# Kernel optimization log

Measured on AMD Instinct MI355X. Metric: run time of the kernel, lower is better.

The kernel has to match this reference:

```python
import jax, jax.numpy as jnp
import numpy as np

B, S, HID = 2, 1024, 1024
H, P, D = 16, 2, 64
SCALE = 1.0 / np.sqrt(D)


def setup_inputs() -> dict:
    key = jax.random.key(0)
    ks = jax.random.split(key, 9)
    hidden_states = jax.random.normal(ks[0], (B, S, HID), dtype=jnp.float32)
    w_std = 0.02
    Wq = jax.random.normal(ks[1], (HID, HID), dtype=jnp.float32) * w_std
    Wk = jax.random.normal(ks[2], (HID, HID), dtype=jnp.float32) * w_std
    Wv = jax.random.normal(ks[3], (HID, HID), dtype=jnp.float32) * w_std
    Wo = jax.random.normal(ks[4], (HID, HID), dtype=jnp.float32) * w_std
    # alpha_* initialized as identity over heads, broadcast over pseudo dim, plus noise
    ident = jnp.broadcast_to(jnp.eye(H, dtype=jnp.float32)[:, :, None], (H, H, P))
    alpha_q = ident + 0.01 * jax.random.normal(ks[5], (H, H, P), dtype=jnp.float32)
    alpha_k = ident + 0.01 * jax.random.normal(ks[6], (H, H, P), dtype=jnp.float32)
    alpha_v = ident + 0.01 * jax.random.normal(ks[7], (H, H, P), dtype=jnp.float32)
    # collapse: (H, H*P), one-hot picking pseudo-head 0 of each head, plus noise
    collapse = jnp.zeros((H, H * P), dtype=jnp.float32)
    hi = jnp.arange(H)
    collapse = collapse.at[hi, hi * P].set(1.0)
    collapse = collapse + 0.01 * jax.random.normal(ks[8], (H, H * P), dtype=jnp.float32)
    return {"hidden_states": hidden_states, "Wq": Wq, "Wk": Wk, "Wv": Wv, "Wo": Wo,
            "alpha_q": alpha_q, "alpha_k": alpha_k, "alpha_v": alpha_v, "collapse": collapse}


def _iha_forward(x, Wq, Wk, Wv, Wo, alpha_q, alpha_k, alpha_v, collapse):
    b, s, _ = x.shape
    # projections (torch F.linear: x @ W^T), split into heads -> (b, H, s, D)
    def proj(W):
        return jnp.einsum('bse,fe->bsf', x, W).reshape(b, s, H, D).transpose(0, 2, 1, 3)
    q, k, v = proj(Wq), proj(Wk), proj(Wv)
    # head mixing: mhp,bmnd->bhpnd then merge pseudo into virtual seq (b,H,s*P,D)
    def mix_merge(alpha, t):
        t = jnp.einsum('mhp,bmnd->bhpnd', alpha, t)
        return t.transpose(0, 1, 3, 2, 4).reshape(b, H, s * P, D)
    q, k, v = mix_merge(alpha_q, q), mix_merge(alpha_k, k), mix_merge(alpha_v, v)
    # causal SDPA over virtual positions
    sv = s * P
    scores = jnp.einsum('bhqd,bhkd->bhqk', q, k) * jnp.asarray(SCALE, x.dtype)
    vpos = jnp.arange(sv)
    causal = vpos[:, None] >= vpos[None, :]
    scores = jnp.where(causal, scores, jnp.asarray(-jnp.inf, x.dtype))
    probs = jax.nn.softmax(scores, axis=-1)
    attn = jnp.einsum('bhqk,bhkd->bhqd', probs, v)  # (b, H, sv, D)
    # collapse pseudo heads: (b,H,s,P,D) -> (b,s,H*P,D) -> einsum with collapse
    attn = attn.reshape(b, H, s, P, D).transpose(0, 2, 1, 3, 4).reshape(b, s, H * P, D)
    attn = jnp.einsum('ho,bnod->bhnd', collapse, attn)  # (b, H, s, D)
    attn = attn.transpose(0, 2, 1, 3).reshape(b, s, HID)
    return jnp.einsum('bse,fe->bsf', attn, Wo)


def reference(hidden_states, Wq, Wk, Wv, Wo, alpha_q, alpha_k, alpha_v, collapse):
    return _iha_forward(hidden_states, Wq, Wk, Wv, Wo, alpha_q, alpha_k, alpha_v, collapse)
```

## Files before the change

kernel.cpp:

```cpp
#include <hip/hip_runtime.h>
#include <hip/hip_bf16.h>

#define B_    2
#define S_    1024
#define HID_  1024
#define H_    16
#define P_    2
#define D_    64
#define SV_   2048
#define NBH_  32
#define SCALE_LOG2E 0.18033688f

typedef __attribute__((ext_vector_type(8))) short short8;
typedef __attribute__((ext_vector_type(4))) short short4b;
typedef __attribute__((ext_vector_type(4))) float f32x4;

#if __has_builtin(__builtin_amdgcn_exp2f)
#define EXP2(x) __builtin_amdgcn_exp2f(x)
#else
#define EXP2(x) exp2f(x)
#endif

__device__ __forceinline__ unsigned short f2bf(float f) {
  union { float f; unsigned u; } v; v.f = f;
  unsigned r = v.u + 0x7fffu + ((v.u >> 16) & 1u);
  return (unsigned short)(r >> 16);
}
__device__ __forceinline__ unsigned pack_bf2(float a, float b) {
  __hip_bfloat162 h = __float22bfloat162_rn(make_float2(a, b));
  unsigned u; __builtin_memcpy(&u, &h, 4);
  return u;
}

__global__ __launch_bounds__(256) void cast_f32_bf16(
    const float* __restrict__ src, unsigned short* __restrict__ dst, int n4) {
  int i = blockIdx.x * blockDim.x + threadIdx.x;
  int stride = gridDim.x * blockDim.x;
  for (; i < n4; i += stride) {
    float4 v = ((const float4*)src)[i];
    ushort4 o;
    o.x = f2bf(v.x); o.y = f2bf(v.y); o.z = f2bf(v.z); o.w = f2bf(v.w);
    ((ushort4*)dst)[i] = o;
  }
}

__global__ __launch_bounds__(256) void weff_kernel(
    const float* __restrict__ Wq, const float* __restrict__ Wk,
    const float* __restrict__ Wv,
    const float* __restrict__ aq, const float* __restrict__ ak,
    const float* __restrict__ av,
    unsigned short* __restrict__ Weff) {
  __shared__ float Al[16][32];
  const int d = blockIdx.x;
  const int t = blockIdx.y;
  const float* W = (t == 0) ? Wq : ((t == 1) ? Wk : Wv);
  const float* A = (t == 0) ? aq : ((t == 1) ? ak : av);
  const int tid = threadIdx.x;
  for (int idx = tid; idx < 512; idx += 256) Al[idx >> 5][idx & 31] = A[idx];
  __syncthreads();
  const int e = tid * 4;
  float wr[16][4];
#pragma unroll
  for (int m = 0; m < 16; ++m) {
    float4 v = *(const float4*)(W + (size_t)(m * 64 + d) * 1024 + e);
    wr[m][0] = v.x; wr[m][1] = v.y; wr[m][2] = v.z; wr[m][3] = v.w;
  }
  for (int hp = 0; hp < 32; ++hp) {
    float acc0 = 0.f, acc1 = 0.f, acc2 = 0.f, acc3 = 0.f;
#pragma unroll
    for (int m = 0; m < 16; ++m) {
      float al = Al[m][hp];
      acc0 += al * wr[m][0]; acc1 += al * wr[m][1];
      acc2 += al * wr[m][2]; acc3 += al * wr[m][3];
    }
    int r = (hp >> 1) * 128 + (hp & 1) * 64 + d;
    ushort4 ov;
    ov.x = f2bf(acc0); ov.y = f2bf(acc1); ov.z = f2bf(acc2); ov.w = f2bf(acc3);
    *(ushort4*)(Weff + ((size_t)t * 2048 + r) * 1024 + e) = ov;
  }
}

__global__ __launch_bounds__(256) void woeff_kernel(
    const float* __restrict__ Wo, const float* __restrict__ coll,
    unsigned short* __restrict__ Woeff) {
  __shared__ float wrow[1024];
  __shared__ float cl[512];
  const int f = blockIdx.x;
  const int tid = threadIdx.x;
  for (int idx = tid; idx < 512; idx += 256) cl[idx] = coll[idx];
  for (int idx = tid; idx < 1024; idx += 256) wrow[idx] = Wo[(size_t)f * 1024 + idx];
  __syncthreads();
  for (int idx = tid; idx < 2048; idx += 256) {
    int o = idx >> 6, d = idx & 63;
    float acc = 0.f;
#pragma unroll
    for (int h = 0; h < 16; ++h) acc += wrow[h * 64 + d] * cl[h * 32 + o];
    Woeff[(size_t)f * 2048 + idx] = f2bf(acc);
  }
}

__global__ __launch_bounds__(512) void qkv_gemm256(
    const unsigned short* __restrict__ Xb,
    const unsigned short* __restrict__ Weff,
    unsigned short* __restrict__ Qd, unsigned short* __restrict__ Kd,
    unsigned short* __restrict__ Vd) {
  __shared__ unsigned short As[3][256 * 64];
  __shared__ unsigned short Bs[2][256 * 64];
  constexpr int K = 1024;
  constexpr int NT = 16;
  const int t = threadIdx.x;
  const int wave = t >> 6, lane = t & 63, lrow = lane & 15, quad = lane >> 4;
  const int wm = wave >> 2, wn = wave & 3;
  const int z = blockIdx.z;
  const int row0 = blockIdx.x * 256, col0 = blockIdx.y * 256;
  const unsigned short* Ap = (z == 2) ? (Weff + (size_t)2 * 2048 * 1024) : Xb;
  const unsigned short* Bp = (z == 2) ? Xb : (Weff + (size_t)z * 2048 * 1024);

  const int srow8 = lane >> 3;
  const int sslot = (lane & 7) ^ srow8;

  auto stageHT = [&](const unsigned short* __restrict__ gsrc,
                     unsigned short* __restrict__ ldsbase,
                     int half, int kt, int trow0) {
#pragma unroll
    for (int j = 0; j < 2; ++j) {
      const int rloc = half * 128 + wave * 16 + j * 8;
      const unsigned short* g =
          gsrc + (size_t)(trow0 + rloc + srow8) * K + kt * 64 + sslot * 8;
      __builtin_amdgcn_global_load_lds(
          (const __attribute__((address_space(1))) unsigned int*)g,
          (__attribute__((address_space(3))) unsigned int*)(ldsbase + rloc * 64),
          16, 0, 0);
    }
  };

  f32x4 acc[8][4];
#pragma unroll
  for (int mi = 0; mi < 8; ++mi)
#pragma unroll
    for (int ni = 0; ni < 4; ++ni) acc[mi][ni] = (f32x4){0.f, 0.f, 0.f, 0.f};

  stageHT(Ap, &As[0][0], 0, 0, row0);
  stageHT(Ap, &As[0][0], 1, 0, row0);
  stageHT(Bp, &Bs[0][0], 0, 0, col0);
  stageHT(Bp, &Bs[0][0], 1, 0, col0);
  stageHT(Ap, &As[1][0], 0, 1, row0);
  stageHT(Ap, &As[1][0], 1, 1, row0);
  stageHT(Bp, &Bs[1][0], 0, 1, col0);
  stageHT(Bp, &Bs[1][0], 1, 1, col0);
  asm volatile("s_waitcnt vmcnt(8)" ::: "memory");
  asm volatile("s_barrier" ::: "memory");

  const int swz = lrow & 7;

#define LDA(mi, ks)                                                         \
  (*(const short8*)(Ab + (wm * 128 + (mi)*16 + lrow) * 64 +                 \
                    ((((ks)*4 + quad) ^ swz) * 8)))

#define MFMA_PAIR(mA, mB, a00, a01, a10, a11)                               \
  _Pragma("unroll") for (int ni = 0; ni < 4; ++ni) {                        \
    acc[mA][ni] = __builtin_amdgcn_mfma_f32_16x16x32_bf16(                  \
        a00, bfrag[ni][0], acc[mA][ni], 0, 0, 0);                           \
    acc[mA][ni] = __builtin_amdgcn_mfma_f32_16x16x32_bf16(                  \
        a01, bfrag[ni][1], acc[mA][ni], 0, 0, 0);                           \
    acc[mB][ni] = __builtin_amdgcn_mfma_f32_16x16x32_bf16(                  \
        a10, bfrag[ni][0], acc[mB][ni], 0, 0, 0);                           \
    acc[mB][ni] = __builtin_amdgcn_mfma_f32_16x16x32_bf16(                  \
        a11, bfrag[ni][1], acc[mB][ni], 0, 0, 0);                           \
  }

  for (int kt = 0; kt < NT; ++kt) {
    const int abuf = kt % 3;
    const int anext = (kt + 2) % 3;
    const int bbuf = kt & 1;
    const bool pf = (kt + 2 < NT);
    const unsigned short* __restrict__ Ab = &As[abuf][0];
    const unsigned short* __restrict__ Bb = &Bs[bbuf][0];

    short8 bfrag[4][2];
    {
#pragma unroll
      for (int ni = 0; ni < 4; ++ni) {
        const int R = wn * 64 + ni * 16 + lrow;
#pragma unroll
        for (int ks = 0; ks < 2; ++ks)
          bfrag[ni][ks] =
              *(const short8*)(Bb + R * 64 + (((ks * 4 + quad) ^ swz) * 8));
      }
      short8 a00 = LDA(0, 0), a01 = LDA(0, 1), a10 = LDA(1, 0), a11 = LDA(1, 1);
      if (pf) stageHT(Ap, &As[anext][0], 0, kt + 2, row0);
      asm volatile("s_barrier" ::: "memory");
      asm volatile("s_waitcnt lgkmcnt(0)" ::: "memory");
      __builtin_amdgcn_s_setprio(1);
      MFMA_PAIR(0, 1, a00, a01, a10, a11)
      __builtin_amdgcn_s_setprio(0);
      asm volatile("s_barrier" ::: "memory");
    }
    {
      short8 a00 = LDA(2, 0), a01 = LDA(2, 1), a10 = LDA(3, 0), a11 = LDA(3, 1);
      if (pf) stageHT(Ap, &As[anext][0], 1, kt + 2, row0);
      asm volatile("s_barrier" ::: "memory");
      asm volatile("s_waitcnt lgkmcnt(0)" ::: "memory");
      __builtin_amdgcn_s_setprio(1);
      MFMA_PAIR(2, 3, a00, a01, a10, a11)
      __builtin_amdgcn_s_setprio(0);
      asm volatile("s_barrier" ::: "memory");
    }
    {
      short8 a00 = LDA(4, 0), a01 = LDA(4, 1), a10 = LDA(5, 0), a11 = LDA(5, 1);
      if (pf) stageHT(Bp, &Bs[bbuf][0], 0, kt + 2, col0);
      asm volatile("s_barrier" ::: "memory");
      asm volatile("s_waitcnt lgkmcnt(0)" ::: "memory");
      __builtin_amdgcn_s_setprio(1);
      MFMA_PAIR(4, 5, a00, a01, a10, a11)
      __builtin_amdgcn_s_setprio(0);
      asm volatile("s_barrier" ::: "memory");
    }
    {
      short8 a00 = LDA(6, 0), a01 = LDA(6, 1), a10 = LDA(7, 0), a11 = LDA(7, 1);
      if (pf) stageHT(Bp, &Bs[bbuf][0], 1, kt + 2, col0);
      asm volatile("s_barrier" ::: "memory");
      asm volatile("s_waitcnt lgkmcnt(0)" ::: "memory");
      __builtin_amdgcn_s_setprio(1);
      MFMA_PAIR(6, 7, a00, a01, a10, a11)
      __builtin_amdgcn_s_setprio(0);
      if (pf) {
        asm volatile("s_waitcnt vmcnt(8)" ::: "memory");
      } else {
        asm volatile("s_waitcnt vmcnt(0)" ::: "memory");
      }
      asm volatile("s_barrier" ::: "memory");
    }
  }
#undef LDA
#undef MFMA_PAIR

#pragma unroll
  for (int mi = 0; mi < 8; ++mi) {
#pragma unroll
    for (int ni = 0; ni < 4; ++ni) {
#pragma unroll
      for (int i = 0; i < 4; ++i) {
        int grow = row0 + wm * 128 + mi * 16 + quad * 4 + i;
        int gcol = col0 + wn * 64 + ni * 16 + lrow;
        float val = acc[mi][ni][i];
        if (z != 2) {
          if (z == 0) val *= SCALE_LOG2E;
          int b = grow >> 10, n = grow & 1023;
          int h = gcol >> 7, p = (gcol >> 6) & 1, d = gcol & 63;
          unsigned short* dst = (z == 0) ? Qd : Kd;
          dst[((size_t)((b * 16 + h) * 2048) + n * 2 + p) * 64 + d] = f2bf(val);
        } else {
          int h = grow >> 7, p = (grow >> 6) & 1, d = grow & 63;
          int b = gcol >> 10, n = gcol & 1023;
          Vd[((size_t)((b * 16 + h) * 64 + d)) * 2048 + n * 2 + p] = f2bf(val);
        }
      }
    }
  }
}

__global__ __launch_bounds__(256) void gemm64p(
    const unsigned short* __restrict__ A,
    const unsigned short* __restrict__ Bbase,
    float* __restrict__ Cf) {
  __shared__ unsigned short As[3][64 * 64];
  __shared__ unsigned short Bs[3][64 * 64];
  constexpr int K = 2048, N = 1024, NT = 32;
  const int t = threadIdx.x;
  const int wave = t >> 6, lane = t & 63, lrow = lane & 15, quad = lane >> 4;
  const int wm = wave >> 1, wn = wave & 1;
  const int row0 = blockIdx.x * 64, col0 = blockIdx.y * 64;
  const int srow8 = lane >> 3;
  const int sslot = (lane & 7) ^ srow8;
  const int swz = lrow & 7;

  auto stage = [&](int kt, int buf) {
#pragma unroll
    for (int j = 0; j < 2; ++j) {
      const int rloc = wave * 16 + j * 8;
      const unsigned short* ga =
          A + (size_t)(row0 + rloc + srow8) * K + kt * 64 + sslot * 8;
      __builtin_amdgcn_global_load_lds(
          (const __attribute__((address_space(1))) unsigned int*)ga,
          (__attribute__((address_space(3))) unsigned int*)(&As[buf][rloc * 64]),
          16, 0, 0);
      const unsigned short* gb =
          Bbase + (size_t)(col0 + rloc + srow8) * K + kt * 64 + sslot * 8;
      __builtin_amdgcn_global_load_lds(
          (const __attribute__((address_space(1))) unsigned int*)gb,
          (__attribute__((address_space(3))) unsigned int*)(&Bs[buf][rloc * 64]),
          16, 0, 0);
    }
  };

  f32x4 acc[2][2];
#pragma unroll
  for (int mi = 0; mi < 2; ++mi)
#pragma unroll
    for (int ni = 0; ni < 2; ++ni) acc[mi][ni] = (f32x4){0.f, 0.f, 0.f, 0.f};

  stage(0, 0);
  stage(1, 1);

  for (int kt = 0; kt < NT; ++kt) {
    const int buf = kt % 3;
    if (kt < NT - 1) {
      asm volatile("s_waitcnt vmcnt(4)" ::: "memory");
    } else {
      asm volatile("s_waitcnt vmcnt(0)" ::: "memory");
    }
    asm volatile("s_barrier" ::: "memory");
    if (kt + 2 < NT) stage(kt + 2, (kt + 2) % 3);

    const unsigned short* __restrict__ Ab = &As[buf][0];
    const unsigned short* __restrict__ Bb = &Bs[buf][0];
    short8 af[2][2], bf[2][2];
#pragma unroll
    for (int mi = 0; mi < 2; ++mi)
#pragma unroll
      for (int ks = 0; ks < 2; ++ks)
        af[mi][ks] = *(const short8*)(
            Ab + (wm * 32 + mi * 16 + lrow) * 64 + (((ks * 4 + quad) ^ swz) * 8));
#pragma unroll
    for (int ni = 0; ni < 2; ++ni)
#pragma unroll
      for (int ks = 0; ks < 2; ++ks)
        bf[ni][ks] = *(const short8*)(
            Bb + (wn * 32 + ni * 16 + lrow) * 64 + (((ks * 4 + quad) ^ swz) * 8));
    __builtin_amdgcn_s_setprio(1);
#pragma unroll
    for (int mi = 0; mi < 2; ++mi)
#pragma unroll
      for (int ni = 0; ni < 2; ++ni) {
        acc[mi][ni] = __builtin_amdgcn_mfma_f32_16x16x32_bf16(
            af[mi][0], bf[ni][0], acc[mi][ni], 0, 0, 0);
        acc[mi][ni] = __builtin_amdgcn_mfma_f32_16x16x32_bf16(
            af[mi][1], bf[ni][1], acc[mi][ni], 0, 0, 0);
      }
    __builtin_amdgcn_s_setprio(0);
  }

#pragma unroll
  for (int mi = 0; mi < 2; ++mi)
#pragma unroll
    for (int ni = 0; ni < 2; ++ni)
#pragma unroll
      for (int i = 0; i < 4; ++i) {
        int grow = row0 + wm * 32 + mi * 16 + quad * 4 + i;
        int gcol = col0 + wn * 32 + ni * 16 + lrow;
        Cf[(size_t)grow * N + gcol] = acc[mi][ni][i];
      }
}

__global__ __launch_bounds__(256, 3) void attn_kernel(
    const unsigned short* __restrict__ Qv, const unsigned short* __restrict__ Kv,
    const unsigned short* __restrict__ Vt, unsigned short* __restrict__ Aov) {
  __shared__ unsigned short Ks[3][4096];
  __shared__ unsigned short Vs[3][4096];
  const int bh = blockIdx.x;
  const int yy = blockIdx.y;
  const int qt = (yy < 16) ? yy : (47 - yy);
  const int t = threadIdx.x;
  const int w = t >> 6, lane = t & 63, lq = lane & 15, quad = lane >> 4;
  const int l3 = lq & 7;

  const unsigned short* Qh = Qv + (size_t)bh * SV_ * D_;
  const unsigned short* Kh = Kv + (size_t)bh * SV_ * D_;
  const unsigned short* Vh = Vt + (size_t)bh * D_ * SV_;

  const int qrow = qt * 64 + w * 16 + lq;
  short8 bq0 = *(const short8*)(Qh + (size_t)qrow * 64 + quad * 8);
  short8 bq1 = *(const short8*)(Qh + (size_t)qrow * 64 + 32 + quad * 8);

  const int sg = (lane & 7) ^ ((lane >> 3) & 7);
  const int r0 = w * 16 + (lane >> 3);
  const unsigned short* Kg0 = Kh + r0 * 64 + sg * 8;
  const unsigned short* Vg0 = Vh + (size_t)r0 * SV_ + sg * 8;
  const int lds0 = w * 1024;
  const int lds1 = lds0 + 512;

  auto stage = [&](int kt) {
    const int buf = kt % 3;
    const unsigned short* kg = Kg0 + kt * 4096;
    const unsigned short* vg = Vg0 + kt * 64;
    __builtin_amdgcn_global_load_lds(
        (const __attribute__((address_space(1))) unsigned int*)kg,
        (__attribute__((address_space(3))) unsigned int*)(&Ks[buf][lds0]), 16, 0, 0);
    __builtin_amdgcn_global_load_lds(
        (const __attribute__((address_space(1))) unsigned int*)(kg + 8 * 64),
        (__attribute__((address_space(3))) unsigned int*)(&Ks[buf][lds1]), 16, 0, 0);
    __builtin_amdgcn_global_load_lds(
        (const __attribute__((address_space(1))) unsigned int*)vg,
        (__attribute__((address_space(3))) unsigned int*)(&Vs[buf][lds0]), 16, 0, 0);
    __builtin_amdgcn_global_load_lds(
        (const __attribute__((address_space(1))) unsigned int*)(vg + (size_t)8 * SV_),
        (__attribute__((address_space(3))) unsigned int*)(&Vs[buf][lds1]), 16, 0, 0);
  };

  float l_sum = 0.f;
  f32x4 o_acc[4];
#pragma unroll
  for (int nd = 0; nd < 4; ++nd) o_acc[nd] = (f32x4){0.f, 0.f, 0.f, 0.f};

  const int nt = qt + 1;
  stage(0);
  if (nt > 1) stage(1);

  for (int kt = 0; kt < nt; ++kt) {
    const int buf = kt % 3;
    if (kt + 1 < nt) {
      asm volatile("s_waitcnt vmcnt(4)" ::: "memory");
    } else {
      asm volatile("s_waitcnt vmcnt(0)" ::: "memory");
    }
    asm volatile("s_barrier" ::: "memory");
    if (kt + 2 < nt) stage(kt + 2);

    const unsigned short* Kb = Ks[buf];
    short8 ka[4][2];
#pragma unroll
    for (int t4 = 0; t4 < 4; ++t4)
#pragma unroll
      for (int c = 0; c < 2; ++c)
        ka[t4][c] = *(const short8*)(Kb + (t4 * 16 + lq) * 64 + (((c * 4 + quad) ^ l3) * 8));

    f32x4 s[4];
#pragma unroll
    for (int t4 = 0; t4 < 4; ++t4) {
      f32x4 z = (f32x4){0.f, 0.f, 0.f, 0.f};
      z = __builtin_amdgcn_mfma_f32_16x16x32_bf16(ka[t4][0], bq0, z, 0, 0, 0);
      s[t4] = __builtin_amdgcn_mfma_f32_16x16x32_bf16(ka[t4][1], bq1, z, 0, 0, 0);
    }

    const bool diag = (kt == qt);
    const int kc0 = kt * 64 + quad * 4;
    const unsigned short* Vb = Vs[buf];
    float rs = 0.f;
    __builtin_amdgcn_s_setprio(1);
#pragma unroll
    for (int t4 = 0; t4 < 4; ++t4) {
      float p0 = EXP2(s[t4][0]), p1 = EXP2(s[t4][1]);
      float p2 = EXP2(s[t4][2]), p3 = EXP2(s[t4][3]);
      if (diag) {
        const int kc = kc0 + t4 * 16;
        if (kc + 0 > qrow) p0 = 0.f;
        if (kc + 1 > qrow) p1 = 0.f;
        if (kc + 2 > qrow) p2 = 0.f;
        if (kc + 3 > qrow) p3 = 0.f;
      }
      rs += (p0 + p1) + (p2 + p3);
      unsigned ww[2];
      ww[0] = pack_bf2(p0, p1);
      ww[1] = pack_bf2(p2, p3);
      short4b pb;
      __builtin_memcpy(&pb, ww, 8);
      const int cg = t4 * 2 + (quad >> 1);
      const int vcol = ((cg ^ l3) * 8) + (quad & 1) * 4;
#pragma unroll
      for (int nd = 0; nd < 4; ++nd) {
        short4b va4;
        __builtin_memcpy(&va4, Vb + (nd * 16 + lq) * 64 + vcol, 8);
        o_acc[nd] = __builtin_amdgcn_mfma_f32_16x16x16bf16_1k(va4, pb,
                                                              o_acc[nd], 0, 0, 0);
      }
    }
    __builtin_amdgcn_s_setprio(0);
    l_sum += rs;
  }

  l_sum += __shfl_xor(l_sum, 16);
  l_sum += __shfl_xor(l_sum, 32);

  const int b = bh >> 4, h = bh & 15;
  const float inv = 1.0f / l_sum;
  const int n = qrow >> 1, p = qrow & 1;
  unsigned short* dst = Aov + ((size_t)(b * 1024 + n)) * 2048 + (h * 2 + p) * 64;
#pragma unroll
  for (int nd = 0; nd < 4; ++nd) {
    uint2 dw;
    dw.x = pack_bf2(o_acc[nd][0] * inv, o_acc[nd][1] * inv);
    dw.y = pack_bf2(o_acc[nd][2] * inv, o_acc[nd][3] * inv);
    *(uint2*)(dst + nd * 16 + quad * 4) = dw;
  }
}

extern "C" void kernel_launch(void* const* d_in, const int* in_sizes, int n_in,
                              void* d_out, int out_size, void* d_ws, size_t ws_size,
                              hipStream_t stream) {
  (void)in_sizes; (void)n_in; (void)out_size; (void)ws_size;
  const float* x    = (const float*)d_in[0];
  const float* Wq   = (const float*)d_in[1];
  const float* Wk   = (const float*)d_in[2];
  const float* Wv   = (const float*)d_in[3];
  const float* Wo   = (const float*)d_in[4];
  const float* aq   = (const float*)d_in[5];
  const float* ak   = (const float*)d_in[6];
  const float* av   = (const float*)d_in[7];
  const float* coll = (const float*)d_in[8];
  float* out = (float*)d_out;

  char* ws = (char*)d_ws;
  const size_t MB = 1024 * 1024;
  unsigned short* Xb    = (unsigned short*)(ws);
  unsigned short* Woeff = (unsigned short*)(ws + 4 * MB);
  unsigned short* Weff  = (unsigned short*)(ws + 8 * MB);
  unsigned short* Qv    = (unsigned short*)(ws + 20 * MB);
  unsigned short* Kv    = (unsigned short*)(ws + 28 * MB);
  unsigned short* Vt    = (unsigned short*)(ws + 36 * MB);
  unsigned short* Aov   = (unsigned short*)(ws + 8 * MB);

  cast_f32_bf16<<<dim3(1024), dim3(256), 0, stream>>>(x, Xb, (B_ * S_ * HID_) / 4);
  weff_kernel<<<dim3(64, 3), dim3(256), 0, stream>>>(Wq, Wk, Wv, aq, ak, av, Weff);
  qkv_gemm256<<<dim3(8, 8, 3), dim3(512), 0, stream>>>(Xb, Weff, Qv, Kv, Vt);
  attn_kernel<<<dim3(32, 32), dim3(256), 0, stream>>>(Qv, Kv, Vt, Aov);
  woeff_kernel<<<dim3(1024), dim3(256), 0, stream>>>(Wo, coll, Woeff);
  gemm64p<<<dim3(32, 16), dim3(256), 0, stream>>>(Aov, Woeff, out);
}
```

Before: 194.9 us.

## Replace 256x256 QKV GEMM with 128x128 tiles and simpler triple-buffered pipeline

The fused QKV projection GEMM drops its 256x256-tile, 512-thread kernel with a split-phase schedule. The replacement uses 128x128 tiles with K-step 32, 256 threads, and a single-barrier triple-buffered global_load_lds pipeline, with a new XOR swizzle for the 32-wide rows. The grid grows from 192 to 768 blocks to fill the 256 CUs more evenly and allow several blocks per CU. In exchange, per-block data reuse falls, so global and LDS traffic rise, and each K-step runs fewer MFMAs per barrier.

Result: faster. 190.5 us (-2.3%).

```diff
diff --git a/kernel.cpp b/kernel.cpp
--- a/kernel.cpp
+++ b/kernel.cpp
@@ -99,150 +99,94 @@
   }
 }
 
-__global__ __launch_bounds__(512) void qkv_gemm256(
+__global__ __launch_bounds__(256, 3) void qkv_gemm128(
     const unsigned short* __restrict__ Xb,
     const unsigned short* __restrict__ Weff,
     unsigned short* __restrict__ Qd, unsigned short* __restrict__ Kd,
     unsigned short* __restrict__ Vd) {
-  __shared__ unsigned short As[3][256 * 64];
-  __shared__ unsigned short Bs[2][256 * 64];
-  constexpr int K = 1024;
-  constexpr int NT = 16;
+  __shared__ unsigned short As[3][128 * 32];
+  __shared__ unsigned short Bs[3][128 * 32];
+  constexpr int K = 1024, NT = 32;
   const int t = threadIdx.x;
-  const int wave = t >> 6, lane = t & 63, lrow = lane & 15, quad = lane >> 4;
-  const int wm = wave >> 2, wn = wave & 3;
+  const int wave = t >> 6, lane = t & 63, lq = lane & 15, quad = lane >> 4;
+  const int wm = wave >> 1, wn = wave & 1;
   const int z = blockIdx.z;
-  const int row0 = blockIdx.x * 256, col0 = blockIdx.y * 256;
+  const int row0 = blockIdx.x * 128, col0 = blockIdx.y * 128;
   const unsigned short* Ap = (z == 2) ? (Weff + (size_t)2 * 2048 * 1024) : Xb;
   const unsigned short* Bp = (z == 2) ? Xb : (Weff + (size_t)z * 2048 * 1024);
 
-  const int srow8 = lane >> 3;
-  const int sslot = (lane & 7) ^ srow8;
-
-  auto stageHT = [&](const unsigned short* __restrict__ gsrc,
-                     unsigned short* __restrict__ ldsbase,
-                     int half, int kt, int trow0) {
+  const int srow = lane >> 2;
+  const int sgr = (lane & 3) ^ ((lane >> 3) & 3);
+
+  auto stage = [&](int kt, int buf) {
 #pragma unroll
     for (int j = 0; j < 2; ++j) {
-      const int rloc = half * 128 + wave * 16 + j * 8;
-      const unsigned short* g =
-          gsrc + (size_t)(trow0 + rloc + srow8) * K + kt * 64 + sslot * 8;
+      const int rloc = wave * 32 + j * 16;
+      const unsigned short* ga =
+          Ap + (size_t)(row0 + rloc + srow) * K + kt * 32 + sgr * 8;
       __builtin_amdgcn_global_load_lds(
-          (const __attribute__((address_space(1))) unsigned int*)g,
-          (__attribute__((address_space(3))) unsigned int*)(ldsbase + rloc * 64),
+          (const __attribute__((address_space(1))) unsigned int*)ga,
+          (__attribute__((address_space(3))) unsigned int*)(&As[buf][rloc * 32]),
           16, 0, 0);
+      const unsigned short* gb =
+          Bp + (size_t)(col0 + rloc + srow) * K + kt * 32 + sgr * 8;
+      __builtin_amdgcn_global_load_lds(
+          (const __attribute__((address_space(1))) unsigned int*)gb,
+          (__attribute__((address_space(3))) unsigned int*)(&Bs[buf][rloc * 32]),
+          16, 0, 0);
     }
   };
 
-  f32x4 acc[8][4];
-#pragma unroll
-  for (int mi = 0; mi < 8; ++mi)
+  f32x4 acc[4][4];
+#pragma unroll
+  for (int mi = 0; mi < 4; ++mi)
 #pragma unroll
     for (int ni = 0; ni < 4; ++ni) acc[mi][ni] = (f32x4){0.f, 0.f, 0.f, 0.f};
 
-  stageHT(Ap, &As[0][0], 0, 0, row0);
-  stageHT(Ap, &As[0][0], 1, 0, row0);
-  stageHT(Bp, &Bs[0][0], 0, 0, col0);
-  stageHT(Bp, &Bs[0][0], 1, 0, col0);
-  stageHT(Ap, &As[1][0], 0, 1, row0);
-  stageHT(Ap, &As[1][0], 1, 1, row0);
-  stageHT(Bp, &Bs[1][0], 0, 1, col0);
-  stageHT(Bp, &Bs[1][0], 1, 1, col0);
-  asm volatile("s_waitcnt vmcnt(8)" ::: "memory");
-  asm volatile("s_barrier" ::: "memory");
-
-  const int swz = lrow & 7;
-
-#define LDA(mi, ks)                                                         \
-  (*(const short8*)(Ab + (wm * 128 + (mi)*16 + lrow) * 64 +                 \
-                    ((((ks)*4 + quad) ^ swz) * 8)))
-
-#define MFMA_PAIR(mA, mB, a00, a01, a10, a11)                               \
-  _Pragma("unroll") for (int ni = 0; ni < 4; ++ni) {                        \
-    acc[mA][ni] = __builtin_amdgcn_mfma_f32_16x16x32_bf16(                  \
-        a00, bfrag[ni][0], acc[mA][ni], 0, 0, 0);                           \
-    acc[mA][ni] = __builtin_amdgcn_mfma_f32_16x16x32_bf16(                  \
-        a01, bfrag[ni][1], acc[mA][ni], 0, 0, 0);                           \
-    acc[mB][ni] = __builtin_amdgcn_mfma_f32_16x16x32_bf16(                  \
-        a10, bfrag[ni][0], acc[mB][ni], 0, 0, 0);                           \
-    acc[mB][ni] = __builtin_amdgcn_mfma_f32_16x16x32_bf16(                  \
-        a11, bfrag[ni][1], acc[mB][ni], 0, 0, 0);                           \
-  }
+  stage(0, 0);
+  stage(1, 1);
+
+  const int swz4 = (lq >> 1) & 3;
 
   for (int kt = 0; kt < NT; ++kt) {
-    const int abuf = kt % 3;
-    const int anext = (kt + 2) % 3;
-    const int bbuf = kt & 1;
-    const bool pf = (kt + 2 < NT);
-    const unsigned short* __restrict__ Ab = &As[abuf][0];
-    const unsigned short* __restrict__ Bb = &Bs[bbuf][0];
-
-    short8 bfrag[4][2];
-    {
-#pragma unroll
-      for (int ni = 0; ni < 4; ++ni) {
-        const int R = wn * 64 + ni * 16 + lrow;
-#pragma unroll
-        for (int ks = 0; ks < 2; ++ks)
-          bfrag[ni][ks] =
-              *(const short8*)(Bb + R * 64 + (((ks * 4 + quad) ^ swz) * 8));
-      }
-      short8 a00 = LDA(0, 0), a01 = LDA(0, 1), a10 = LDA(1, 0), a11 = LDA(1, 1);
-      if (pf) stageHT(Ap, &As[anext][0], 0, kt + 2, row0);
-      asm volatile("s_barrier" ::: "memory");
-      asm volatile("s_waitcnt lgkmcnt(0)" ::: "memory");
-      __builtin_amdgcn_s_setprio(1);
-      MFMA_PAIR(0, 1, a00, a01, a10, a11)
-      __builtin_amdgcn_s_setprio(0);
-      asm volatile("s_barrier" ::: "memory");
-    }
-    {
-      short8 a00 = LDA(2, 0), a01 = LDA(2, 1), a10 = LDA(3, 0), a11 = LDA(3, 1);
-      if (pf) stageHT(Ap, &As[anext][0], 1, kt + 2, row0);
-      asm volatile("s_barrier" ::: "memory");
-      asm volatile("s_waitcnt lgkmcnt(0)" ::: "memory");
-      __builtin_amdgcn_s_setprio(1);
-      MFMA_PAIR(2, 3, a00, a01, a10, a11)
-      __builtin_amdgcn_s_setprio(0);
-      asm volatile("s_barrier" ::: "memory");
-    }
-    {
-      short8 a00 = LDA(4, 0), a01 = LDA(4, 1), a10 = LDA(5, 0), a11 = LDA(5, 1);
-      if (pf) stageHT(Bp, &Bs[bbuf][0], 0, kt + 2, col0);
-      asm volatile("s_barrier" ::: "memory");
-      asm volatile("s_waitcnt lgkmcnt(0)" ::: "memory");
-      __builtin_amdgcn_s_setprio(1);
-      MFMA_PAIR(4, 5, a00, a01, a10, a11)
-      __builtin_amdgcn_s_setprio(0);
-      asm volatile("s_barrier" ::: "memory");
-    }
-    {
-      short8 a00 = LDA(6, 0), a01 = LDA(6, 1), a10 = LDA(7, 0), a11 = LDA(7, 1);
-      if (pf) stageHT(Bp, &Bs[bbuf][0], 1, kt + 2, col0);
-      asm volatile("s_barrier" ::: "memory");
-      asm volatile("s_waitcnt lgkmcnt(0)" ::: "memory");
-      __builtin_amdgcn_s_setprio(1);
-      MFMA_PAIR(6, 7, a00, a01, a10, a11)
-      __builtin_amdgcn_s_setprio(0);
-      if (pf) {
-        asm volatile("s_waitcnt vmcnt(8)" ::: "memory");
-      } else {
-        asm volatile("s_waitcnt vmcnt(0)" ::: "memory");
-      }
-      asm volatile("s_barrier" ::: "memory");
-    }
-  }
-#undef LDA
-#undef MFMA_PAIR
-
-#pragma unroll
-  for (int mi = 0; mi < 8; ++mi) {
+    const int buf = kt % 3;
+    if (kt + 1 < NT) {
+      asm volatile("s_waitcnt vmcnt(4)" ::: "memory");
+    } else {
+      asm volatile("s_waitcnt vmcnt(0)" ::: "memory");
+    }
+    asm volatile("s_barrier" ::: "memory");
+    if (kt + 2 < NT) stage(kt + 2, (kt + 2) % 3);
+
+    const unsigned short* __restrict__ Ab = &As[buf][0];
+    const unsigned short* __restrict__ Bb = &Bs[buf][0];
+    short8 af[4], bf[4];
+#pragma unroll
+    for (int mi = 0; mi < 4; ++mi)
+      af[mi] = *(const short8*)(
+          Ab + (wm * 64 + mi * 16 + lq) * 32 + ((quad ^ swz4) * 8));
+#pragma unroll
+    for (int ni = 0; ni < 4; ++ni)
+      bf[ni] = *(const short8*)(
+          Bb + (wn * 64 + ni * 16 + lq) * 32 + ((quad ^ swz4) * 8));
+    __builtin_amdgcn_s_setprio(1);
+#pragma unroll
+    for (int mi = 0; mi < 4; ++mi)
+#pragma unroll
+      for (int ni = 0; ni < 4; ++ni)
+        acc[mi][ni] = __builtin_amdgcn_mfma_f32_16x16x32_bf16(
+            af[mi], bf[ni], acc[mi][ni], 0, 0, 0);
+    __builtin_amdgcn_s_setprio(0);
+  }
+
+#pragma unroll
+  for (int mi = 0; mi < 4; ++mi) {
 #pragma unroll
     for (int ni = 0; ni < 4; ++ni) {
 #pragma unroll
       for (int i = 0; i < 4; ++i) {
-        int grow = row0 + wm * 128 + mi * 16 + quad * 4 + i;
-        int gcol = col0 + wn * 64 + ni * 16 + lrow;
+        int grow = row0 + wm * 64 + mi * 16 + quad * 4 + i;
+        int gcol = col0 + wn * 64 + ni * 16 + lq;
         float val = acc[mi][ni][i];
         if (z != 2) {
           if (z == 0) val *= SCALE_LOG2E;
@@ -512,7 +456,7 @@
 
   cast_f32_bf16<<<dim3(1024), dim3(256), 0, stream>>>(x, Xb, (B_ * S_ * HID_) / 4);
   weff_kernel<<<dim3(64, 3), dim3(256), 0, stream>>>(Wq, Wk, Wv, aq, ak, av, Weff);
-  qkv_gemm256<<<dim3(8, 8, 3), dim3(512), 0, stream>>>(Xb, Weff, Qv, Kv, Vt);
+  qkv_gemm128<<<dim3(16, 16, 3), dim3(256), 0, stream>>>(Xb, Weff, Qv, Kv, Vt);
   attn_kernel<<<dim3(32, 32), dim3(256), 0, stream>>>(Qv, Kv, Vt, Aov);
   woeff_kernel<<<dim3(1024), dim3(256), 0, stream>>>(Wo, coll, Woeff);
   gemm64p<<<dim3(32, 16), dim3(256), 0, stream>>>(Aov, Woeff, out);
```
